# Performance work log

Hardware: AMD Instinct MI355X
Metric: run time of the kernel (lower is better)

## Reference

```python
import jax, jax.numpy as jnp
import numpy as np

B, N, T, C, H = 8, 325, 12, 128, 8
D = C // H
TIME_NUM, FE = 288, 4


def _ln(x, g, b):
    m = jnp.mean(x, -1, keepdims=True)
    v = jnp.mean((x - m) ** 2, -1, keepdims=True)
    return (x - m) * jax.lax.rsqrt(v + 1e-5) * g + b


def setup_inputs() -> dict:
    rk = jax.random.key(0)
    ks = iter(jax.random.split(rk, 64))
    n = lambda *s: jax.random.normal(next(ks), s, dtype=jnp.float32) * 0.02
    inp = dict(
        query=jax.random.normal(next(ks), (B, N, T, C), dtype=jnp.float32),
        key=jax.random.normal(next(ks), (B, N, T, C), dtype=jnp.float32),
        value=jax.random.normal(next(ks), (B, N, T, C), dtype=jnp.float32),
        adj=jax.random.uniform(next(ks), (N, N), dtype=jnp.float32),
        D_S=jax.random.uniform(next(ks), (N, N), dtype=jnp.float32),
        Ws_emb=n(N, C), bs_emb=n(C),
        Wq_s=n(D, D), Wk_s=n(D, D), Wv_s=n(D, D),
        Wfc_s=n(C, C), bfc_s=n(C),
        g1s=jnp.ones(C, jnp.float32), be1s=jnp.zeros(C, jnp.float32),
        g2s=jnp.ones(C, jnp.float32), be2s=jnp.zeros(C, jnp.float32),
        W1s=n(C, FE * C), bf1s=n(FE * C), W2s=n(FE * C, C), bf2s=n(C),
        Wg1=n(C, 2 * C), bg1=n(2 * C), Wg2=n(2 * C, C), bg2=n(C),
        Wfs=n(C, C), bfs=n(C), Wfg=n(C, C), bfg=n(C),
        Temb=n(TIME_NUM, C),
        Wq_t=n(D, D), bq_t=n(D), Wk_t=n(D, D), bk_t=n(D), Wv_t=n(D, D), bv_t=n(D),
        Wfc_t=n(C, C), bfc_t=n(C),
        g1t=jnp.ones(C, jnp.float32), be1t=jnp.zeros(C, jnp.float32),
        g2t=jnp.ones(C, jnp.float32), be2t=jnp.zeros(C, jnp.float32),
        W1t=n(C, FE * C), bf1t=n(FE * C), W2t=n(FE * C, C), bf2t=n(C),
        gb1=jnp.ones(C, jnp.float32), bb1=jnp.zeros(C, jnp.float32),
        gb2=jnp.ones(C, jnp.float32), bb2=jnp.zeros(C, jnp.float32),
        t=0, num_layers=2,
    )
    return inp


def reference(query, key, value, adj, D_S, Ws_emb, bs_emb, Wq_s, Wk_s, Wv_s,
              Wfc_s, bfc_s, g1s, be1s, g2s, be2s, W1s, bf1s, W2s, bf2s,
              Wg1, bg1, Wg2, bg2, Wfs, bfs, Wfg, bfg, Temb,
              Wq_t, bq_t, Wk_t, bk_t, Wv_t, bv_t, Wfc_t, bfc_t,
              g1t, be1t, g2t, be2t, W1t, bf1t, W2t, bf2t,
              gb1, bb1, gb2, bb2, t, num_layers):
    scale = jnp.sqrt(jnp.float32(C))
    # D_S embedding: [N,N] @ [N,C] -> [N,C], broadcast to [B,N,T,C]
    D_S_b = (D_S @ Ws_emb + bs_emb)[None, :, None, :]
    q = k = None
    q, k, v = query, key, value
    a = adj
    out = q
    for _ in range(num_layers):
        # ---- STransformer ----
        # InstanceNorm2d(1) over whole adj; source mutates self.adj so it is
        # re-normalized every layer invocation.
        m = jnp.mean(a)
        va = jnp.mean((a - m) ** 2)
        a = (a - m) * jax.lax.rsqrt(va + 1e-5)
        # GCN on raw q (before D_S is added), batched over (B,T)
        h = jnp.einsum('nm,bmtc->bntc', a, q @ Wg1) + bg1
        h = jax.nn.relu(h)
        h = jnp.einsum('nm,bmtc->bntc', a, h @ Wg2) + bg2
        X_G = jax.nn.log_softmax(h, axis=-1)
        qd = q + D_S_b
        kd = k + D_S_b
        vd = v + D_S_b
        # spatial attention: NOTE source derives queries AND values from the
        # `values` tensor (query arg only supplies shape) - kept faithful.
        vh = vd.reshape(B, N, T, H, D)
        kh = kd.reshape(B, N, T, H, D)
        qs = vh @ Wq_s
        ks_ = kh @ Wk_s
        vs = vh @ Wv_s
        attn = jnp.einsum('bqthd,bkthd->bqkth', qs, ks_)
        att = jax.nn.softmax(attn / scale, axis=1)  # softmax over QUERY axis (faithful)
        o = jnp.einsum('bqkth,bkthd->bqthd', att, vs).reshape(B, N, T, C)
        o = o @ Wfc_s + bfc_s
        M_s = _ln(o + qd, g1s, be1s)
        ff = jax.nn.relu(M_s @ W1s + bf1s) @ W2s + bf2s
        U_s = _ln(ff + M_s, g2s, be2s)
        g = jax.nn.sigmoid(U_s @ Wfs + bfs + X_G @ Wfg + bfg)
        sp = g * U_s + (1.0 - g) * X_G
        out1 = _ln(sp + q, gb1, bb1)
        # ---- TTransformer ----
        x = out1 + Temb[:T][None, None, :, :]
        xh = x.reshape(B, N, T, H, D)
        qt = xh @ Wq_t + bq_t
        kt = xh @ Wk_t + bk_t
        vt = xh @ Wv_t + bv_t
        at = jnp.einsum('bnqhd,bnkhd->bnqkh', qt, kt)
        at = jax.nn.softmax(at / scale, axis=2)  # softmax over QUERY axis (faithful)
        ot = jnp.einsum('bnqkh,bnkhd->bnqhd', at, vt).reshape(B, N, T, C)
        ot = ot @ Wfc_t + bfc_t
        M_t = _ln(ot + x, g1t, be1t)
        fft = jax.nn.relu(M_t @ W1t + bf1t) @ W2t + bf2t
        U_t = _ln(M_t + fft, g2t, be2t)
        tt = U_t + x + M_t
        out = _ln(tt + out1, gb2, bb2)
        q = k = v = out
    return out
```

## Files before the change

### kernel.cpp

```cpp
#include <hip/hip_runtime.h>

#define B_ 8
#define N_ 325
#define T_ 12
#define C_ 128
#define H_ 8
#define NPAD 384
#define BSTR (NPAD * T_ * C_)
#define REAL (N_ * T_ * C_)
#define INV_SCALE 0.08838834764831845f

typedef short bf16x8 __attribute__((ext_vector_type(8)));
typedef short bf16x4 __attribute__((ext_vector_type(4)));
typedef float f32x4 __attribute__((ext_vector_type(4)));

#define MFMA16(a, b, c) __builtin_amdgcn_mfma_f32_16x16x16bf16_1k(a, b, c, 0, 0, 0)

__device__ __forceinline__ unsigned short f2b(float f) {
    unsigned int u = __float_as_uint(f);
    unsigned int r = u + 0x7FFFu + ((u >> 16) & 1u);
    return (unsigned short)(r >> 16);
}
__device__ __forceinline__ float b2f(unsigned short h) {
    return __uint_as_float((unsigned int)h << 16);
}
__device__ __forceinline__ ushort2 fsplit(float v) {
    unsigned short h = f2b(v);
    return make_ushort2(h, f2b(v - b2f(h)));
}
__device__ __forceinline__ float rsum16(float v) {
    #pragma unroll
    for (int m = 1; m <= 8; m <<= 1) v += __shfl_xor(v, m);
    return v;
}

__global__ void splitq_kernel(const float* __restrict__ in, ushort2* __restrict__ out) {
    long i = (long)blockIdx.x * 256 + threadIdx.x;
    long m = i >> 7;
    int c = (int)(i & 127);
    int b = (int)(m / (N_ * T_));
    int rem = (int)(m - (long)b * (N_ * T_));
    out[(long)b * BSTR + (long)rem * 128 + c] = fsplit(in[i]);
}

__global__ void padzero_kernel(ushort2* __restrict__ buf) {
    int i = blockIdx.x * 256 + threadIdx.x;
    const int per = (NPAD - N_) * T_ * C_;
    if (i < B_ * per) {
        int b = i / per, r = i - b * per;
        buf[(long)b * BSTR + REAL + r] = make_ushort2(0, 0);
    }
}

struct WSegs {
    const float* src[10];
    ushort2* dst[10];
    int n[10];
};
__global__ void split_many(WSegs s) {
    int seg = blockIdx.y;
    int i = blockIdx.x * 256 + threadIdx.x;
    if (i < s.n[seg]) s.dst[seg][i] = fsplit(s.src[seg][i]);
}

__global__ void dsb_kernel(const float* __restrict__ DS, const float* __restrict__ Ws,
                           const float* __restrict__ bs, float* __restrict__ dsb) {
    int n = blockIdx.x, c = threadIdx.x;
    float acc = bs[c];
    for (int m = 0; m < N_; m++) acc += DS[n * N_ + m] * Ws[m * C_ + c];
    dsb[n * C_ + c] = acc;
}

__global__ __launch_bounds__(1024) void anorm_part(const float* __restrict__ in, float* __restrict__ part) {
    const int NT = N_ * N_;
    int tid = threadIdx.x;
    long g = (long)blockIdx.x * 1024 + tid;
    float s = 0.f, s2 = 0.f;
    for (long i = g; i < NT; i += (long)gridDim.x * 1024) { float v = in[i]; s += v; s2 += v * v; }
    __shared__ float r1[1024], r2[1024];
    r1[tid] = s; r2[tid] = s2; __syncthreads();
    for (int k = 512; k > 0; k >>= 1) {
        if (tid < k) { r1[tid] += r1[tid + k]; r2[tid] += r2[tid + k]; }
        __syncthreads();
    }
    if (tid == 0) { part[blockIdx.x * 2] = r1[0]; part[blockIdx.x * 2 + 1] = r2[0]; }
}
__global__ __launch_bounds__(256) void anorm_fin(const float* __restrict__ in, const float* __restrict__ part,
                                                 float* __restrict__ out, ushort2* __restrict__ outsp) {
    const int NT = N_ * N_;
    float S = 0.f, S2 = 0.f;
    for (int j = 0; j < 104; j++) { S += part[j * 2]; S2 += part[j * 2 + 1]; }
    float mean = S / (float)NT;
    float r = rsqrtf(S2 / (float)NT - mean * mean + 1e-5f);
    int i = blockIdx.x * 256 + threadIdx.x;
    if (i < NT) out[i] = (in[i] - mean) * r;
    if (i < N_ * NPAD) {
        int n = i / NPAD, c = i - n * NPAD;
        outsp[i] = (c < N_) ? fsplit((in[n * N_ + c] - mean) * r) : make_ushort2(0, 0);
    }
}

template<int OUTF, int OUTS, int OUTH, int RELU>
__global__ __launch_bounds__(256) void spgemm(
    const ushort2* __restrict__ Ag, const ushort2* __restrict__ Bg,
    const float* __restrict__ bias, float* __restrict__ Cf, ushort2* __restrict__ Csp,
    unsigned short* __restrict__ Chi,
    int M, int K, int Nout, long sA, long sB, long sC, int biasLen) {
    __shared__ unsigned short Ah[64][72], Al[64][72];
    __shared__ unsigned short Bh[64][72], Bl[64][72];
    int z = blockIdx.z;
    int n0 = blockIdx.x * 64, m0 = blockIdx.y * 64;
    int tid = threadIdx.x;
    int amr = tid >> 2, akg = (tid & 3) << 4;
    int bnn = tid & 63, bkg = (tid >> 6) << 4;
    int w = tid >> 6, l = tid & 63, lm = l & 15, lq = l >> 4;
    bool am_ok = (m0 + amr) < M;
    f32x4 acc[4];
    #pragma unroll
    for (int i = 0; i < 4; i++) acc[i] = (f32x4){0.f, 0.f, 0.f, 0.f};

    for (int k0 = 0; k0 < K; k0 += 64) {
        {
            const ushort2* ap = Ag + sA * z + (long)(m0 + amr) * K + k0 + akg;
            alignas(16) ushort2 e[16];
            if (am_ok) {
                const uint4* p = (const uint4*)ap;
                *(uint4*)&e[0]  = p[0];
                *(uint4*)&e[4]  = p[1];
                *(uint4*)&e[8]  = p[2];
                *(uint4*)&e[12] = p[3];
            } else {
                #pragma unroll
                for (int j = 0; j < 16; j++) e[j] = make_ushort2(0, 0);
            }
            alignas(16) unsigned short hh[16], hl[16];
            #pragma unroll
            for (int j = 0; j < 16; j++) { hh[j] = e[j].x; hl[j] = e[j].y; }
            *(bf16x8*)&Ah[amr][akg]     = *(bf16x8*)&hh[0];
            *(bf16x8*)&Ah[amr][akg + 8] = *(bf16x8*)&hh[8];
            *(bf16x8*)&Al[amr][akg]     = *(bf16x8*)&hl[0];
            *(bf16x8*)&Al[amr][akg + 8] = *(bf16x8*)&hl[8];
        }
        {
            alignas(16) unsigned short hh[16], hl[16];
            #pragma unroll
            for (int r = 0; r < 16; r++) {
                ushort2 e = Bg[sB * z + (long)(k0 + bkg + r) * Nout + n0 + bnn];
                hh[r] = e.x; hl[r] = e.y;
            }
            *(bf16x8*)&Bh[bnn][bkg]     = *(bf16x8*)&hh[0];
            *(bf16x8*)&Bh[bnn][bkg + 8] = *(bf16x8*)&hh[8];
            *(bf16x8*)&Bl[bnn][bkg]     = *(bf16x8*)&hl[0];
            *(bf16x8*)&Bl[bnn][bkg + 8] = *(bf16x8*)&hl[8];
        }
        __syncthreads();
        #pragma unroll
        for (int s = 0; s < 2; s++) {
            bf16x8 ah = *(const bf16x8*)&Ah[w * 16 + lm][s * 32 + lq * 8];
            bf16x8 al = *(const bf16x8*)&Al[w * 16 + lm][s * 32 + lq * 8];
            #pragma unroll
            for (int nt = 0; nt < 4; nt++) {
                bf16x8 bh = *(const bf16x8*)&Bh[nt * 16 + lm][s * 32 + lq * 8];
                bf16x8 bl = *(const bf16x8*)&Bl[nt * 16 + lm][s * 32 + lq * 8];
                acc[nt] = __builtin_amdgcn_mfma_f32_16x16x32_bf16(ah, bh, acc[nt], 0, 0, 0);
                acc[nt] = __builtin_amdgcn_mfma_f32_16x16x32_bf16(ah, bl, acc[nt], 0, 0, 0);
                acc[nt] = __builtin_amdgcn_mfma_f32_16x16x32_bf16(al, bh, acc[nt], 0, 0, 0);
            }
        }
        __syncthreads();
    }
    int mbase = m0 + w * 16 + lq * 4;
    #pragma unroll
    for (int nt = 0; nt < 4; nt++) {
        int n = n0 + nt * 16 + lm;
        float bv = bias ? bias[n % biasLen] : 0.f;
        #pragma unroll
        for (int r = 0; r < 4; r++) {
            int m = mbase + r;
            if (m < M) {
                float v = acc[nt][r] + bv;
                if (RELU) v = fmaxf(v, 0.f);
                long gi = sC * z + (long)m * Nout + n;
                if constexpr (OUTF) Cf[gi] = v;
                if constexpr (OUTS) Csp[gi] = fsplit(v);
                if constexpr (OUTH) Chi[gi] = f2b(v);
            }
        }
    }
}

template<int OUTF, int OUTS, int OUTH, int RELU>
static inline void spg(const ushort2* A, const ushort2* Bw, const float* bias,
                       float* Cf, ushort2* Csp, unsigned short* Chi, int M, int K, int Nout,
                       long sA, long sB, long sC, int biasLen, int batch, hipStream_t stream) {
    dim3 g(Nout / 64, (M + 63) / 64, batch);
    spgemm<OUTF, OUTS, OUTH, RELU><<<g, 256, 0, stream>>>(A, Bw, bias, Cf, Csp, Chi, M, K, Nout, sA, sB, sC, biasLen);
}

template<int EPI, int AHI>
__global__ __launch_bounds__(256) void fgemm(
    const void* __restrict__ Ag, const ushort2* __restrict__ Bg,
    const float* __restrict__ bias, int M, int K,
    const float* __restrict__ R1, const float* __restrict__ nbc, const float* __restrict__ tbc,
    const float* __restrict__ gA, const float* __restrict__ Uf,
    const float* __restrict__ Xf, const float* __restrict__ qf,
    const float* __restrict__ Mres, const float* __restrict__ o1,
    const float* __restrict__ g1, const float* __restrict__ be1,
    const float* __restrict__ gamma, const float* __restrict__ beta,
    float* __restrict__ Outf, ushort2* __restrict__ Outsp) {
    __shared__ unsigned short Ah[64][72], Al[AHI ? 1 : 64][72];
    __shared__ unsigned short Bh[128][72], Bl[128][72];
    int m0 = blockIdx.x * 64;
    int tid = threadIdx.x;
    int amr = tid >> 2, akg = (tid & 3) << 4;
    int bnn = tid & 127, bkg = (tid >> 7) << 5;
    int w = tid >> 6, l = tid & 63, lm = l & 15, lq = l >> 4;
    bool am_ok = (m0 + amr) < M;
    f32x4 acc[8];
    #pragma unroll
    for (int i = 0; i < 8; i++) acc[i] = (f32x4){0.f, 0.f, 0.f, 0.f};

    for (int k0 = 0; k0 < K; k0 += 64) {
        if constexpr (AHI) {
            const unsigned short* ap = (const unsigned short*)Ag + (long)(m0 + amr) * K + k0 + akg;
            if (am_ok) {
                const bf16x8* p = (const bf16x8*)ap;
                *(bf16x8*)&Ah[amr][akg]     = p[0];
                *(bf16x8*)&Ah[amr][akg + 8] = p[1];
            } else {
                bf16x8 zz = {0,0,0,0,0,0,0,0};
                *(bf16x8*)&Ah[amr][akg]     = zz;
                *(bf16x8*)&Ah[amr][akg + 8] = zz;
            }
        } else {
            const ushort2* ap = (const ushort2*)Ag + (long)(m0 + amr) * K + k0 + akg;
            alignas(16) ushort2 e[16];
            if (am_ok) {
                const uint4* p = (const uint4*)ap;
                *(uint4*)&e[0]  = p[0];
                *(uint4*)&e[4]  = p[1];
                *(uint4*)&e[8]  = p[2];
                *(uint4*)&e[12] = p[3];
            } else {
                #pragma unroll
                for (int j = 0; j < 16; j++) e[j] = make_ushort2(0, 0);
            }
            alignas(16) unsigned short hh[16], hl[16];
            #pragma unroll
            for (int j = 0; j < 16; j++) { hh[j] = e[j].x; hl[j] = e[j].y; }
            *(bf16x8*)&Ah[amr][akg]     = *(bf16x8*)&hh[0];
            *(bf16x8*)&Ah[amr][akg + 8] = *(bf16x8*)&hh[8];
            *(bf16x8*)&Al[amr][akg]     = *(bf16x8*)&hl[0];
            *(bf16x8*)&Al[amr][akg + 8] = *(bf16x8*)&hl[8];
        }
        {
            alignas(16) unsigned short hh[32], hl[32];
            #pragma unroll
            for (int r = 0; r < 32; r++) {
                ushort2 e = Bg[(long)(k0 + bkg + r) * 128 + bnn];
                hh[r] = e.x; hl[r] = e.y;
            }
            #pragma unroll
            for (int j = 0; j < 4; j++)
                *(bf16x8*)&Bh[bnn][bkg + 8 * j] = *(bf16x8*)&hh[8 * j];
            #pragma unroll
            for (int j = 0; j < 4; j++)
                *(bf16x8*)&Bl[bnn][bkg + 8 * j] = *(bf16x8*)&hl[8 * j];
        }
        __syncthreads();
        #pragma unroll
        for (int s = 0; s < 2; s++) {
            bf16x8 ah = *(const bf16x8*)&Ah[w * 16 + lm][s * 32 + lq * 8];
            bf16x8 al;
            if constexpr (!AHI) al = *(const bf16x8*)&Al[w * 16 + lm][s * 32 + lq * 8];
            #pragma unroll
            for (int nt = 0; nt < 8; nt++) {
                bf16x8 bh = *(const bf16x8*)&Bh[nt * 16 + lm][s * 32 + lq * 8];
                bf16x8 bl = *(const bf16x8*)&Bl[nt * 16 + lm][s * 32 + lq * 8];
                acc[nt] = __builtin_amdgcn_mfma_f32_16x16x32_bf16(ah, bh, acc[nt], 0, 0, 0);
                acc[nt] = __builtin_amdgcn_mfma_f32_16x16x32_bf16(ah, bl, acc[nt], 0, 0, 0);
                if constexpr (!AHI)
                    acc[nt] = __builtin_amdgcn_mfma_f32_16x16x32_bf16(al, bh, acc[nt], 0, 0, 0);
            }
        }
        __syncthreads();
    }
    int mbase = m0 + w * 16 + lq * 4;
    #pragma unroll
    for (int r = 0; r < 4; r++) {
        int m = mbase + r;
        bool ok = m < M;
        long base = (long)m * 128;
        float vv[8];
        #pragma unroll
        for (int nt = 0; nt < 8; nt++) {
            int col = nt * 16 + lm;
            vv[nt] = acc[nt][r] + bias[col];
        }
        if (ok) {
            if constexpr (EPI == 0) {
                int nr = (m / T_) % N_, tr = m % T_;
                #pragma unroll
                for (int nt = 0; nt < 8; nt++) {
                    int col = nt * 16 + lm;
                    if (R1)  vv[nt] += R1[base + col];
                    if (nbc) vv[nt] += nbc[nr * 128 + col];
                    if (tbc) vv[nt] += tbc[tr * 128 + col];
                }
            } else if constexpr (EPI == 1) {
                #pragma unroll
                for (int nt = 0; nt < 8; nt++) {
                    int col = nt * 16 + lm;
                    float g = 1.f / (1.f + __expf(-(vv[nt] + gA[base + col])));
                    vv[nt] = g * Uf[base + col] + (1.f - g) * Xf[base + col] + qf[base + col];
                }
            } else {
                float mr[8];
                #pragma unroll
                for (int nt = 0; nt < 8; nt++) {
                    mr[nt] = Mres[base + nt * 16 + lm];
                    vv[nt] += mr[nt];
                }
                float s = 0.f;
                #pragma unroll
                for (int nt = 0; nt < 8; nt++) s += vv[nt];
                s = rsum16(s);
                float mean = s * (1.f / 128);
                float var = 0.f;
                #pragma unroll
                for (int nt = 0; nt < 8; nt++) { float d = vv[nt] - mean; var += d * d; }
                var = rsum16(var);
                float rr = rsqrtf(var * (1.f / 128) + 1e-5f);
                int tr = m % T_;
                #pragma unroll
                for (int nt = 0; nt < 8; nt++) {
                    int col = nt * 16 + lm;
                    float u = (vv[nt] - mean) * rr * g1[col] + be1[col];
                    vv[nt] = u + mr[nt] + 2.f * o1[base + col] + tbc[tr * 128 + col];
                }
            }
            float s = 0.f;
            #pragma unroll
            for (int nt = 0; nt < 8; nt++) s += vv[nt];
            s = rsum16(s);
            float mean = s * (1.f / 128);
            float var = 0.f;
            #pragma unroll
            for (int nt = 0; nt < 8; nt++) { float d = vv[nt] - mean; var += d * d; }
            var = rsum16(var);
            float rr = rsqrtf(var * (1.f / 128) + 1e-5f);
            long spb = base;
            if constexpr (EPI == 2) {
                int b = m / (N_ * T_);
                int rem = m - b * (N_ * T_);
                spb = (long)b * BSTR + (long)rem * 128;
            }
            #pragma unroll
            for (int nt = 0; nt < 8; nt++) {
                int col = nt * 16 + lm;
                float o = (vv[nt] - mean) * rr * gamma[col] + beta[col];
                if (Outf) Outf[base + col] = o;
                if (Outsp) Outsp[spb + col] = fsplit(o);
            }
        }
    }
}

__global__ __launch_bounds__(256) void lsm_kernel(const float* __restrict__ in, float* __restrict__ out,
                                                  ushort2* __restrict__ outsp) {
    int lane = threadIdx.x & 63;
    long token = (long)blockIdx.x * 4 + (threadIdx.x >> 6);
    long base = token * C_;
    float v0 = in[base + lane], v1 = in[base + lane + 64];
    float m = fmaxf(v0, v1);
    #pragma unroll
    for (int o = 32; o; o >>= 1) m = fmaxf(m, __shfl_xor(m, o));
    float e = __expf(v0 - m) + __expf(v1 - m);
    #pragma unroll
    for (int o = 32; o; o >>= 1) e += __shfl_xor(e, o);
    float lz = __logf(e);
    float o0 = v0 - m - lz, o1 = v1 - m - lz;
    out[base + lane] = o0;
    out[base + lane + 64] = o1;
    outsp[base + lane] = fsplit(o0);
    outsp[base + lane + 64] = fsplit(o1);
}

#define QT16 21
__global__ __launch_bounds__(256) void satt_kernel(
    const float* __restrict__ Vt, const float* __restrict__ Kt, const float* __restrict__ dsb,
    const float* __restrict__ Wq, const float* __restrict__ Wk, const float* __restrict__ Wv,
    ushort2* __restrict__ O) {
    int bid = blockIdx.x;
    int h = bid & 7;
    int t = (bid >> 3) % T_;
    int b = bid / (T_ * H_);
    __shared__ unsigned short Qb[336 * 20];
    __shared__ unsigned short Kb[336 * 20];
    __shared__ unsigned short Vb[16 * 340];
    __shared__ float rZ[336];
    __shared__ unsigned short Esc[4][16 * 20];
    int tid = threadIdx.x;
    int w = tid >> 6, l = tid & 63, lm = l & 15, lq = l >> 4;

    for (int i = tid; i < 11 * 20; i += 256) { Qb[325 * 20 + i] = 0; Kb[325 * 20 + i] = 0; }
    bf16x4 bWq, bWk, bWv;
    {
        alignas(8) unsigned short wq[4], wk[4], wv[4];
        #pragma unroll
        for (int jj = 0; jj < 4; jj++) {
            int j = lq * 4 + jj;
            wq[jj] = f2b(Wq[j * 16 + lm] * INV_SCALE);
            wk[jj] = f2b(Wk[j * 16 + lm]);
            wv[jj] = f2b(Wv[j * 16 + lm]);
        }
        bWq = *(bf16x4*)wq; bWk = *(bf16x4*)wk; bWv = *(bf16x4*)wv;
    }
    for (int idx = tid; idx < N_ * 4; idx += 256) {
        int n = idx >> 2, c4 = idx & 3;
        long rb = (((long)b * N_ + n) * T_ + t) * C_ + h * 16 + c4 * 4;
        f32x4 v4 = *(const f32x4*)&Vt[rb];
        f32x4 k4 = *(const f32x4*)&Kt[rb];
        f32x4 d4 = *(const f32x4*)&dsb[n * C_ + h * 16 + c4 * 4];
        alignas(8) unsigned short hv[4], hk[4];
        #pragma unroll
        for (int e = 0; e < 4; e++) { hv[e] = f2b(v4[e] + d4[e]); hk[e] = f2b(k4[e] + d4[e]); }
        *(bf16x4*)&Qb[n * 20 + c4 * 4] = *(bf16x4*)hv;
        *(bf16x4*)&Kb[n * 20 + c4 * 4] = *(bf16x4*)hk;
    }
    __syncthreads();
    for (int nt = w; nt < QT16; nt += 4) {
        bf16x4 av = *(const bf16x4*)&Qb[(nt * 16 + lm) * 20 + lq * 4];
        bf16x4 ak = *(const bf16x4*)&Kb[(nt * 16 + lm) * 20 + lq * 4];
        f32x4 zz = (f32x4){0.f, 0.f, 0.f, 0.f};
        f32x4 qs = MFMA16(av, bWq, zz);
        f32x4 ks = MFMA16(ak, bWk, zz);
        f32x4 vs = MFMA16(av, bWv, zz);
        #pragma unroll
        for (int r = 0; r < 4; r++) {
            int row = nt * 16 + lq * 4 + r;
            Qb[row * 20 + lm] = f2b(qs[r]);
            Kb[row * 20 + lm] = f2b(ks[r]);
            Vb[lm * 340 + row] = f2b(vs[r]);
        }
    }
    __syncthreads();
    for (int kt = w; kt < QT16; kt += 4) {
        bf16x4 bk = *(const bf16x4*)&Kb[(kt * 16 + lm) * 20 + lq * 4];
        float zacc = 0.f;
        for (int qt = 0; qt < QT16; qt++) {
            bf16x4 aq = *(const bf16x4*)&Qb[(qt * 16 + lm) * 20 + lq * 4];
            f32x4 sv = MFMA16(aq, bk, ((f32x4){0.f, 0.f, 0.f, 0.f}));
            int qbase = qt * 16 + lq * 4;
            #pragma unroll
            for (int r = 0; r < 4; r++) {
                float e = __expf(sv[r]);
                zacc += (qbase + r < N_) ? e : 0.f;
            }
        }
        zacc += __shfl_xor(zacc, 16);
        zacc += __shfl_xor(zacc, 32);
        int k = kt * 16 + lm;
        if (lq == 0) rZ[k] = (k < N_) ? 1.f / zacc : 0.f;
    }
    __syncthreads();
    unsigned short* esc = &Esc[w][0];
    for (int qt = w; qt < QT16; qt += 4) {
        bf16x4 aq = *(const bf16x4*)&Qb[(qt * 16 + lm) * 20 + lq * 4];
        f32x4 acc = (f32x4){0.f, 0.f, 0.f, 0.f};
        for (int kt = 0; kt < QT16; kt++) {
            bf16x4 bk = *(const bf16x4*)&Kb[(kt * 16 + lm) * 20 + lq * 4];
            f32x4 sv = MFMA16(aq, bk, ((f32x4){0.f, 0.f, 0.f, 0.f}));
            float rz = rZ[kt * 16 + lm];
            #pragma unroll
            for (int r = 0; r < 4; r++) {
                float e = __expf(sv[r]) * rz;
                esc[(lq * 4 + r) * 20 + lm] = (unsigned short)(__float_as_uint(e) >> 16);
            }
            __asm__ __volatile__("s_waitcnt lgkmcnt(0)" ::: "memory");
            bf16x4 ef = *(const bf16x4*)&esc[lm * 20 + lq * 4];
            bf16x4 vf = *(const bf16x4*)&Vb[lm * 340 + kt * 16 + lq * 4];
            acc = MFMA16(ef, vf, acc);
            __asm__ __volatile__("s_waitcnt lgkmcnt(0)" ::: "memory");
        }
        #pragma unroll
        for (int r = 0; r < 4; r++) {
            int q = qt * 16 + lq * 4 + r;
            if (q < N_) O[(((long)b * N_ + q) * T_ + t) * C_ + h * 16 + lm] = fsplit(acc[r]);
        }
    }
}

__global__ __launch_bounds__(128) void tatt_kernel(
    const float* __restrict__ out1, const float* __restrict__ Temb,
    const float* __restrict__ Wq, const float* __restrict__ bq,
    const float* __restrict__ Wk, const float* __restrict__ bk,
    const float* __restrict__ Wv, const float* __restrict__ bv,
    ushort2* __restrict__ O) {
    int bid = blockIdx.x;
    int n = bid % N_;
    int b = bid / N_;
    int tid = threadIdx.x;
    __shared__ float xl[T_ * C_];
    __shared__ float qt[T_ * C_], kt[T_ * C_], vt[T_ * C_];
    __shared__ float sl[T_ * T_ * H_];
    __shared__ float wql[256], wkl[256], wvl[256], bql[16], bkl[16], bvl[16];
    if (tid < 16) { bql[tid] = bq[tid]; bkl[tid] = bk[tid]; bvl[tid] = bv[tid]; }
    for (int i = tid; i < 256; i += 128) { wql[i] = Wq[i]; wkl[i] = Wk[i]; wvl[i] = Wv[i]; }
    for (int i = tid; i < T_ * C_; i += 128) {
        int t = i >> 7, c = i & 127;
        xl[i] = out1[(((long)b * N_ + n) * T_ + t) * C_ + c] + Temb[t * C_ + c];
    }
    __syncthreads();
    for (int i = tid; i < T_ * C_; i += 128) {
        int t = i >> 7, c = i & 127;
        int h16 = c & ~15, d = c & 15;
        float aq = bql[d], ak = bkl[d], av = bvl[d];
        #pragma unroll
        for (int j = 0; j < 16; j++) {
            float x = xl[t * C_ + h16 + j];
            aq += x * wql[j * 16 + d];
            ak += x * wkl[j * 16 + d];
            av += x * wvl[j * 16 + d];
        }
        qt[i] = aq; kt[i] = ak; vt[i] = av;
    }
    __syncthreads();
    for (int i = tid; i < T_ * T_ * H_; i += 128) {
        int h = i & 7;
        int k = (i >> 3) % T_;
        int q = i / (T_ * H_);
        float s = 0.f;
        #pragma unroll
        for (int d = 0; d < 16; d++) s += qt[q * C_ + h * 16 + d] * kt[k * C_ + h * 16 + d];
        sl[(q * T_ + k) * H_ + h] = s * INV_SCALE;
    }
    __syncthreads();
    if (tid < T_ * H_) {
        int k = tid >> 3, h = tid & 7;
        float m = -1e30f;
        for (int q = 0; q < T_; q++) m = fmaxf(m, sl[(q * T_ + k) * H_ + h]);
        float Z = 0.f;
        for (int q = 0; q < T_; q++) Z += __expf(sl[(q * T_ + k) * H_ + h] - m);
        float rZi = 1.f / Z;
        for (int q = 0; q < T_; q++) sl[(q * T_ + k) * H_ + h] = __expf(sl[(q * T_ + k) * H_ + h] - m) * rZi;
    }
    __syncthreads();
    for (int i = tid; i < T_ * C_; i += 128) {
        int t = i >> 7, c = i & 127;
        int h = c >> 4, d = c & 15;
        float acc = 0.f;
        #pragma unroll
        for (int k = 0; k < T_; k++) acc += sl[(t * T_ + k) * H_ + h] * vt[k * C_ + h * 16 + d];
        O[(((long)b * N_ + n) * T_ + t) * C_ + c] = fsplit(acc);
    }
}

extern "C" void kernel_launch(void* const* d_in, const int* in_sizes, int n_in,
                              void* d_out, int out_size, void* d_ws, size_t ws_size,
                              hipStream_t stream) {
    const float* query  = (const float*)d_in[0];
    const float* key_   = (const float*)d_in[1];
    const float* value  = (const float*)d_in[2];
    const float* adj    = (const float*)d_in[3];
    const float* D_S    = (const float*)d_in[4];
    const float* Ws_emb = (const float*)d_in[5];
    const float* bs_emb = (const float*)d_in[6];
    const float* Wq_s   = (const float*)d_in[7];
    const float* Wk_s   = (const float*)d_in[8];
    const float* Wv_s   = (const float*)d_in[9];
    const float* Wfc_s  = (const float*)d_in[10];
    const float* bfc_s  = (const float*)d_in[11];
    const float* g1s    = (const float*)d_in[12];
    const float* be1s   = (const float*)d_in[13];
    const float* g2s    = (const float*)d_in[14];
    const float* be2s   = (const float*)d_in[15];
    const float* W1s    = (const float*)d_in[16];
    const float* bf1s   = (const float*)d_in[17];
    const float* W2s    = (const float*)d_in[18];
    const float* bf2s   = (const float*)d_in[19];
    const float* Wg1    = (const float*)d_in[20];
    const float* bg1    = (const float*)d_in[21];
    const float* Wg2    = (const float*)d_in[22];
    const float* bg2    = (const float*)d_in[23];
    const float* Wfs    = (const float*)d_in[24];
    const float* bfs    = (const float*)d_in[25];
    const float* Wfg    = (const float*)d_in[26];
    const float* bfg    = (const float*)d_in[27];
    const float* Temb   = (const float*)d_in[28];
    const float* Wq_t   = (const float*)d_in[29];
    const float* bq_t   = (const float*)d_in[30];
    const float* Wk_t   = (const float*)d_in[31];
    const float* bk_t   = (const float*)d_in[32];
    const float* Wv_t   = (const float*)d_in[33];
    const float* bv_t   = (const float*)d_in[34];
    const float* Wfc_t  = (const float*)d_in[35];
    const float* bfc_t  = (const float*)d_in[36];
    const float* g1t    = (const float*)d_in[37];
    const float* be1t   = (const float*)d_in[38];
    const float* g2t    = (const float*)d_in[39];
    const float* be2t   = (const float*)d_in[40];
    const float* W1t    = (const float*)d_in[41];
    const float* bf1t   = (const float*)d_in[42];
    const float* W2t    = (const float*)d_in[43];
    const float* bf2t   = (const float*)d_in[44];
    const float* gb1    = (const float*)d_in[45];
    const float* bb1    = (const float*)d_in[46];
    const float* gb2    = (const float*)d_in[47];
    const float* bb2    = (const float*)d_in[48];

    float* out = (float*)d_out;
    float* ws = (float*)d_ws;
    const long SZ = (long)B_ * N_ * T_ * C_;
    const int M_tok = B_ * N_ * T_;
    float* dsb   = ws;
    float* anorm = ws + 41600;
    float* apart = ws + 41600 + 105632;
    float* xg = apart + 256;
    float* tB = xg + SZ;
    float* tC = tB + SZ;
    float* tD = tC + SZ;
    float* p = tD + SZ;
    ushort2* anorm_sp = (ushort2*)p;
    ushort2* q_sp = (ushort2*)(p + 124832);
    float* alias4 = p + 124832 + 4718592;
    ushort2* aggq  = (ushort2*)alias4;
    ushort2* t0sp  = (ushort2*)(alias4 + SZ);
    ushort2* tAsp  = (ushort2*)(alias4 + 3 * SZ);
    unsigned short* hidhi = (unsigned short*)alias4;
    float* tAf     = alias4;
    float* p2 = alias4 + 4 * SZ;
    ushort2* tBsp = (ushort2*)p2;
    ushort2* tCsp = (ushort2*)(p2 + SZ);
    ushort2* t1sp = (ushort2*)p2;
    ushort2* xgsp = (ushort2*)(p2 + 2 * SZ);
    ushort2* wsp  = (ushort2*)(p2 + 3 * SZ);
    ushort2* Wg1sp   = wsp;
    ushort2* Wg2sp   = wsp + 32768;
    ushort2* Wfcs_sp = wsp + 65536;
    ushort2* W1s_sp  = wsp + 81920;
    ushort2* W2s_sp  = wsp + 147456;
    ushort2* Wfs_sp  = wsp + 212992;
    ushort2* Wfg_sp  = wsp + 229376;
    ushort2* Wfct_sp = wsp + 245760;
    ushort2* W1t_sp  = wsp + 262144;
    ushort2* W2t_sp  = wsp + 327680;

    const int LNG = M_tok / 4;
    const int PZG = (B_ * (NPAD - N_) * T_ * C_ + 255) / 256;

    dsb_kernel<<<dim3(N_), dim3(128), 0, stream>>>(D_S, Ws_emb, bs_emb, dsb);
    splitq_kernel<<<dim3((int)(SZ / 256)), 256, 0, stream>>>(query, q_sp);
    padzero_kernel<<<PZG, 256, 0, stream>>>(q_sp);
    anorm_part<<<104, 1024, 0, stream>>>(adj, apart);
    anorm_fin<<<488, 256, 0, stream>>>(adj, apart, anorm, anorm_sp);
    {
        WSegs s;
        const float* srcs[10] = {Wg1, Wg2, Wfc_s, W1s, W2s, Wfs, Wfg, Wfc_t, W1t, W2t};
        ushort2* dsts[10] = {Wg1sp, Wg2sp, Wfcs_sp, W1s_sp, W2s_sp, Wfs_sp, Wfg_sp, Wfct_sp, W1t_sp, W2t_sp};
        int ns[10] = {32768, 32768, 16384, 65536, 65536, 16384, 16384, 16384, 65536, 65536};
        for (int i = 0; i < 10; i++) { s.src[i] = srcs[i]; s.dst[i] = dsts[i]; s.n[i] = ns[i]; }
        split_many<<<dim3(256, 10), 256, 0, stream>>>(s);
    }

    for (int lay = 0; lay < 2; lay++) {
        const float* q  = lay ? out : query;
        const float* kk = lay ? out : key_;
        const float* vv = lay ? out : value;
        const float* z = nullptr;
        padzero_kernel<<<PZG, 256, 0, stream>>>(t1sp);
        spg<0,1,0,0>(anorm_sp, q_sp, nullptr, nullptr, aggq, nullptr, N_, NPAD, 1536, 0, BSTR, REAL, 1536, 8, stream);
        spg<0,1,0,1>(aggq, Wg1sp, bg1, nullptr, t0sp, nullptr, N_ * T_, 128, 256, REAL, 0, (long)N_ * T_ * 256, 256, 8, stream);
        spg<0,1,0,0>(t0sp, Wg2sp, nullptr, nullptr, t1sp, nullptr, N_ * T_, 256, 128, (long)N_ * T_ * 256, 0, BSTR, 128, 8, stream);
        spg<1,0,0,0>(anorm_sp, t1sp, bg2, tB, nullptr, nullptr, N_, NPAD, 1536, 0, BSTR, REAL, 128, 8, stream);
        lsm_kernel<<<LNG, 256, 0, stream>>>(tB, xg, xgsp);
        satt_kernel<<<B_ * T_ * H_, 256, 0, stream>>>(vv, kk, dsb, Wq_s, Wk_s, Wv_s, tAsp);
        fgemm<0,0><<<488, 256, 0, stream>>>(tAsp, Wfcs_sp, bfc_s, M_tok, 128,
            q, dsb, z, z, z, z, z, z, z, z, z, g1s, be1s, tC, tCsp);
        spg<0,0,1,1>(tCsp, W1s_sp, bf1s, nullptr, nullptr, hidhi, M_tok, 128, 512, 0, 0, 0, 512, 1, stream);
        fgemm<0,1><<<488, 256, 0, stream>>>(hidhi, W2s_sp, bf2s, M_tok, 512,
            tC, z, z, z, z, z, z, z, z, z, z, g2s, be2s, tB, tBsp);
        spg<1,0,0,0>(tBsp, Wfs_sp, bfs, tAf, nullptr, nullptr, M_tok, 128, 128, 0, 0, 0, 128, 1, stream);
        fgemm<1,0><<<488, 256, 0, stream>>>(xgsp, Wfg_sp, bfg, M_tok, 128,
            z, z, z, tAf, tB, xg, q, z, z, z, z, gb1, bb1, tD, nullptr);
        tatt_kernel<<<B_ * N_, 128, 0, stream>>>(tD, Temb, Wq_t, bq_t, Wk_t, bk_t, Wv_t, bv_t, tAsp);
        fgemm<0,0><<<488, 256, 0, stream>>>(tAsp, Wfct_sp, bfc_t, M_tok, 128,
            tD, z, Temb, z, z, z, z, z, z, z, z, g1t, be1t, tC, tCsp);
        spg<0,0,1,1>(tCsp, W1t_sp, bf1t, nullptr, nullptr, hidhi, M_tok, 128, 512, 0, 0, 0, 512, 1, stream);
        fgemm<2,1><<<488, 256, 0, stream>>>(hidhi, W2t_sp, bf2t, M_tok, 512,
            z, z, Temb, z, z, z, z, tC, tD, g2t, be2t, gb2, bb2, out, q_sp);
    }
}
```

Baseline: 1.132 ms.

## Fold softmax normalizer into V and compute transposed scores to drop LDS staging

The spatial attention kernel now scales V by the per-key reciprocal normalizer once, then computes transposed scores (K·Q) so the exponentiated tile already sits in the register layout the P·V MFMA needs. This removes the per-tile LDS round trip through the Esc scratch buffer and its explicit waitcnt barriers. The normalizer loop drops the per-element validity mask and instead subtracts 11, which is exp(0) from each zero-padded query row. The P·V loop also alternates two accumulators to shorten the MFMA dependency chain, and outputs are written with 16-byte vector stores. Rounding V·rZ to bf16 adds one extra rounding step, and the subtract-11 trick relies on the padded Q rows being exactly zero.

```diff
diff --git a/kernel.cpp b/kernel.cpp
--- a/kernel.cpp
+++ b/kernel.cpp
@@ -399,7 +399,6 @@
     __shared__ unsigned short Kb[336 * 20];
     __shared__ unsigned short Vb[16 * 340];
     __shared__ float rZ[336];
-    __shared__ unsigned short Esc[4][16 * 20];
     int tid = threadIdx.x;
     int w = tid >> 6, l = tid & 63, lm = l & 15, lq = l >> 4;
 
@@ -451,42 +450,40 @@
         for (int qt = 0; qt < QT16; qt++) {
             bf16x4 aq = *(const bf16x4*)&Qb[(qt * 16 + lm) * 20 + lq * 4];
             f32x4 sv = MFMA16(aq, bk, ((f32x4){0.f, 0.f, 0.f, 0.f}));
-            int qbase = qt * 16 + lq * 4;
-            #pragma unroll
-            for (int r = 0; r < 4; r++) {
-                float e = __expf(sv[r]);
-                zacc += (qbase + r < N_) ? e : 0.f;
-            }
+            zacc += __expf(sv[0]) + __expf(sv[1]) + __expf(sv[2]) + __expf(sv[3]);
         }
         zacc += __shfl_xor(zacc, 16);
         zacc += __shfl_xor(zacc, 32);
         int k = kt * 16 + lm;
-        if (lq == 0) rZ[k] = (k < N_) ? 1.f / zacc : 0.f;
-    }
-    __syncthreads();
-    unsigned short* esc = &Esc[w][0];
+        if (lq == 0) rZ[k] = (k < N_) ? 1.f / (zacc - 11.f) : 0.f;
+    }
+    __syncthreads();
+    for (int i = tid; i < 16 * 336; i += 256) {
+        int d = i / 336, k = i - d * 336;
+        Vb[d * 340 + k] = f2b(b2f(Vb[d * 340 + k]) * rZ[k]);
+    }
+    __syncthreads();
     for (int qt = w; qt < QT16; qt += 4) {
-        bf16x4 aq = *(const bf16x4*)&Qb[(qt * 16 + lm) * 20 + lq * 4];
-        f32x4 acc = (f32x4){0.f, 0.f, 0.f, 0.f};
-        for (int kt = 0; kt < QT16; kt++) {
-            bf16x4 bk = *(const bf16x4*)&Kb[(kt * 16 + lm) * 20 + lq * 4];
-            f32x4 sv = MFMA16(aq, bk, ((f32x4){0.f, 0.f, 0.f, 0.f}));
-            float rz = rZ[kt * 16 + lm];
-            #pragma unroll
-            for (int r = 0; r < 4; r++) {
-                float e = __expf(sv[r]) * rz;
-                esc[(lq * 4 + r) * 20 + lm] = (unsigned short)(__float_as_uint(e) >> 16);
-            }
-            __asm__ __volatile__("s_waitcnt lgkmcnt(0)" ::: "memory");
-            bf16x4 ef = *(const bf16x4*)&esc[lm * 20 + lq * 4];
-            bf16x4 vf = *(const bf16x4*)&Vb[lm * 340 + kt * 16 + lq * 4];
-            acc = MFMA16(ef, vf, acc);
-            __asm__ __volatile__("s_waitcnt lgkmcnt(0)" ::: "memory");
-        }
-        #pragma unroll
-        for (int r = 0; r < 4; r++) {
-            int q = qt * 16 + lq * 4 + r;
-            if (q < N_) O[(((long)b * N_ + q) * T_ + t) * C_ + h * 16 + lm] = fsplit(acc[r]);
+        bf16x4 bq = *(const bf16x4*)&Qb[(qt * 16 + lm) * 20 + lq * 4];
+        f32x4 accA = (f32x4){0.f, 0.f, 0.f, 0.f};
+        f32x4 accB = (f32x4){0.f, 0.f, 0.f, 0.f};
+        auto pv = [&](int kt, f32x4 a) -> f32x4 {
+            bf16x4 ak = *(const bf16x4*)&Kb[(kt * 16 + lm) * 20 + lq * 4];
+            f32x4 sv = MFMA16(ak, bq, ((f32x4){0.f, 0.f, 0.f, 0.f}));
+            alignas(8) unsigned short eh[4];
+            #pragma unroll
+            for (int r = 0; r < 4; r++) eh[r] = f2b(__expf(sv[r]));
+            bf16x4 av = *(const bf16x4*)&Vb[lm * 340 + kt * 16 + lq * 4];
+            return MFMA16(av, *(bf16x4*)eh, a);
+        };
+        for (int kt = 0; kt < QT16 - 1; kt += 2) { accA = pv(kt, accA); accB = pv(kt + 1, accB); }
+        accA = pv(QT16 - 1, accA);
+        int q = qt * 16 + lm;
+        if (q < N_) {
+            alignas(16) ushort2 o4[4];
+            #pragma unroll
+            for (int r = 0; r < 4; r++) o4[r] = fsplit(accA[r] + accB[r]);
+            *(uint4*)&O[(((long)b * N_ + q) * T_ + t) * C_ + h * 16 + lq * 4] = *(const uint4*)o4;
         }
     }
 }
```

After: 1.119 ms. About the same (-1.1%).
